# Kernel optimization log

Hardware: AMD Instinct MI355X
Metric: run time of the kernel (lower is better)

Reference implementation:

```python
import jax, jax.numpy as jnp
import numpy as np

B, T, J, D = 64, 800, 50, 200  # batch, context len, query len, 2*hidden

def setup_inputs() -> dict:
    key = jax.random.key(0)
    ks = jax.random.split(key, 8)
    return {
        'h':    jax.random.normal(ks[0], (B, T, D), jnp.float32),
        'u':    jax.random.normal(ks[1], (B, J, D), jnp.float32),
        'w_h':  jax.random.normal(ks[2], (D,), jnp.float32) * 0.05,
        'b_h':  jax.random.normal(ks[3], (1,), jnp.float32) * 0.05,
        'w_u':  jax.random.normal(ks[4], (D,), jnp.float32) * 0.05,
        'b_u':  jax.random.normal(ks[5], (1,), jnp.float32) * 0.05,
        'w_hu': jax.random.normal(ks[6], (D,), jnp.float32) * 0.05,
        'b_hu': jax.random.normal(ks[7], (1,), jnp.float32) * 0.05,
    }

def reference(h, u, w_h, b_h, w_u, b_u, w_hu, b_hu):
    # Similarity: s[b,t,j] = ws_h(h_t) + ws_u(u_j) + ws_hu(h_t * u_j)  (+ summed biases)
    # Computed without materializing the [B,T,J,D] expanded tensors of the original.
    sh = jnp.einsum('btd,d->bt', h, w_h)            # [B,T]
    su = jnp.einsum('bjd,d->bj', u, w_u)            # [B,J]
    shu = jnp.einsum('btd,bjd->btj', h * w_hu, u)   # [B,T,J]
    s = shu + sh[:, :, None] + su[:, None, :] + (b_h + b_u + b_hu)[0]
    # Context-to-query attention
    a = jax.nn.softmax(s, axis=2)                   # [B,T,J]
    c2q = jnp.einsum('btj,bjd->btd', a, u)          # [B,T,D]
    # Query-to-context attention
    b = jax.nn.softmax(jnp.max(s, axis=2), axis=1)  # [B,T]
    q2c = jnp.einsum('bt,btd->bd', b, h)[:, None, :]  # [B,1,D], broadcasts over T
    g = jnp.concatenate([h, c2q, h * c2q, h * q2c], axis=-1)  # [B,T,4D]
    return g
```

## Files before the change

kernel.cpp:

```cpp
#include <hip/hip_runtime.h>
#include <cstdint>
#include <cstddef>

#define B_ 64
#define T_ 800
#define J_ 50
#define D_ 200
#define TILE1 100
#define NTILE1 8
#define NW 8
#define TT 5
#define NPASS 20

__device__ __forceinline__ float dot4(float4 a, float4 b) {
    return fmaf(a.x, b.x, fmaf(a.y, b.y, fmaf(a.z, b.z, a.w * b.w)));
}
__device__ __forceinline__ int rotc(int k, int j) {
    int kk = k + ((j >> 2) & 7);
    return (kk >= 50) ? kk - 50 : kk;
}

__global__ __launch_bounds__(512, 4) void k1_kernel(
    const float* __restrict__ h, const float* __restrict__ u,
    const float* __restrict__ w_h, const float* __restrict__ b_h,
    const float* __restrict__ w_u, const float* __restrict__ b_u,
    const float* __restrict__ w_hu, const float* __restrict__ b_hu,
    float* __restrict__ g, float* __restrict__ smax_ws, float* __restrict__ q2c)
{
    __shared__ __align__(16) float4 u4_s[50][50];
    __shared__ __align__(16) float4 hw_s[NW][TT][25];
    __shared__ float a_s[NW][TT][52];

    const int tid  = threadIdx.x;
    const int b    = blockIdx.x >> 3;
    const int tile = blockIdx.x & 7;

    if (tile == 0 && tid < D_) q2c[b * D_ + tid] = 0.f;

    for (int idx = tid; idx < 2500; idx += 512) {
        const int j = idx / 50, k = idx - (idx / 50) * 50;
        u4_s[j][rotc(k, j)] = *reinterpret_cast<const float4*>(&u[(b * J_ + j) * D_ + 4 * k]);
    }
    __syncthreads();

    const int lane = tid & 63;
    const int w    = tid >> 6;
    const int urow = (lane < 50) ? lane : 49;
    const int dcol = (lane < 50) ? lane : 0;

    float4 whu_r = make_float4(0.f, 0.f, 0.f, 0.f);
    float4 wh_r  = make_float4(0.f, 0.f, 0.f, 0.f);
    if (lane < 50) {
        whu_r = *reinterpret_cast<const float4*>(&w_hu[4 * lane]);
        wh_r  = *reinterpret_cast<const float4*>(&w_h[4 * lane]);
    }

    float su = b_h[0] + b_u[0] + b_hu[0];
    #pragma unroll 5
    for (int k = 0; k < 50; ++k) {
        const float4 wu4 = *reinterpret_cast<const float4*>(&w_u[4 * k]);
        su += dot4(u4_s[urow][rotc(k, urow)], wu4);
    }

    for (int p = w; p < NPASS; p += NW) {
        const int t0 = tile * TILE1 + p * TT;

        float4 h4r[TT];
        float  shr[TT];
        #pragma unroll
        for (int tt = 0; tt < TT; ++tt) {
            float4 h4 = make_float4(0.f, 0.f, 0.f, 0.f);
            if (lane < 50)
                h4 = *reinterpret_cast<const float4*>(&h[(size_t)(b * T_ + t0 + tt) * D_ + 4 * lane]);
            h4r[tt] = h4;
            if (lane < 25) {
                float4 hw; hw.x = h4.x * whu_r.x; hw.y = h4.y * whu_r.y;
                hw.z = h4.z * whu_r.z; hw.w = h4.w * whu_r.w;
                hw_s[w][tt][lane] = hw;
            }
            float ps = dot4(h4, wh_r);
            #pragma unroll
            for (int off = 32; off > 0; off >>= 1) ps += __shfl_xor(ps, off);
            shr[tt] = ps;
        }

        float s[TT];
        #pragma unroll
        for (int tt = 0; tt < TT; ++tt) s[tt] = su + shr[tt];

        #pragma unroll 5
        for (int k = 0; k < 25; ++k) {
            const float4 u4 = u4_s[urow][rotc(k, urow)];
            #pragma unroll
            for (int tt = 0; tt < TT; ++tt) s[tt] += dot4(hw_s[w][tt][k], u4);
        }
        #pragma unroll
        for (int tt = 0; tt < TT; ++tt) {
            if (lane >= 25 && lane < 50) {
                float4 hw; hw.x = h4r[tt].x * whu_r.x; hw.y = h4r[tt].y * whu_r.y;
                hw.z = h4r[tt].z * whu_r.z; hw.w = h4r[tt].w * whu_r.w;
                hw_s[w][tt][lane - 25] = hw;
            }
        }
        #pragma unroll 5
        for (int k = 25; k < 50; ++k) {
            const float4 u4 = u4_s[urow][rotc(k, urow)];
            #pragma unroll
            for (int tt = 0; tt < TT; ++tt) s[tt] += dot4(hw_s[w][tt][k - 25], u4);
        }

        #pragma unroll
        for (int tt = 0; tt < TT; ++tt) {
            float m = (lane < J_) ? s[tt] : -3.4e38f;
            #pragma unroll
            for (int off = 32; off > 0; off >>= 1) m = fmaxf(m, __shfl_xor(m, off));
            float e = (lane < J_) ? __expf(s[tt] - m) : 0.f;
            float sum = e;
            #pragma unroll
            for (int off = 32; off > 0; off >>= 1) sum += __shfl_xor(sum, off);
            if (lane < J_) a_s[w][tt][lane] = e / sum;
            if (lane == 0) smax_ws[b * T_ + (t0 + tt)] = m;
        }

        float4 c2q[TT];
        #pragma unroll
        for (int tt = 0; tt < TT; ++tt) c2q[tt] = make_float4(0.f, 0.f, 0.f, 0.f);
        #pragma unroll 3
        for (int j4 = 0; j4 < 12; ++j4) {
            const float4 ua0 = u4_s[4 * j4 + 0][rotc(dcol, 4 * j4 + 0)];
            const float4 ua1 = u4_s[4 * j4 + 1][rotc(dcol, 4 * j4 + 1)];
            const float4 ua2 = u4_s[4 * j4 + 2][rotc(dcol, 4 * j4 + 2)];
            const float4 ua3 = u4_s[4 * j4 + 3][rotc(dcol, 4 * j4 + 3)];
            #pragma unroll
            for (int tt = 0; tt < TT; ++tt) {
                const float4 a4 = *reinterpret_cast<const float4*>(&a_s[w][tt][4 * j4]);
                c2q[tt].x = fmaf(a4.x, ua0.x, c2q[tt].x);
                c2q[tt].y = fmaf(a4.x, ua0.y, c2q[tt].y);
                c2q[tt].z = fmaf(a4.x, ua0.z, c2q[tt].z);
                c2q[tt].w = fmaf(a4.x, ua0.w, c2q[tt].w);
                c2q[tt].x = fmaf(a4.y, ua1.x, c2q[tt].x);
                c2q[tt].y = fmaf(a4.y, ua1.y, c2q[tt].y);
                c2q[tt].z = fmaf(a4.y, ua1.z, c2q[tt].z);
                c2q[tt].w = fmaf(a4.y, ua1.w, c2q[tt].w);
                c2q[tt].x = fmaf(a4.z, ua2.x, c2q[tt].x);
                c2q[tt].y = fmaf(a4.z, ua2.y, c2q[tt].y);
                c2q[tt].z = fmaf(a4.z, ua2.z, c2q[tt].z);
                c2q[tt].w = fmaf(a4.z, ua2.w, c2q[tt].w);
                c2q[tt].x = fmaf(a4.w, ua3.x, c2q[tt].x);
                c2q[tt].y = fmaf(a4.w, ua3.y, c2q[tt].y);
                c2q[tt].z = fmaf(a4.w, ua3.z, c2q[tt].z);
                c2q[tt].w = fmaf(a4.w, ua3.w, c2q[tt].w);
            }
        }
        {
            const float4 ua0 = u4_s[48][rotc(dcol, 48)];
            const float4 ua1 = u4_s[49][rotc(dcol, 49)];
            #pragma unroll
            for (int tt = 0; tt < TT; ++tt) {
                const float a0 = a_s[w][tt][48], a1 = a_s[w][tt][49];
                c2q[tt].x = fmaf(a0, ua0.x, c2q[tt].x);
                c2q[tt].y = fmaf(a0, ua0.y, c2q[tt].y);
                c2q[tt].z = fmaf(a0, ua0.z, c2q[tt].z);
                c2q[tt].w = fmaf(a0, ua0.w, c2q[tt].w);
                c2q[tt].x = fmaf(a1, ua1.x, c2q[tt].x);
                c2q[tt].y = fmaf(a1, ua1.y, c2q[tt].y);
                c2q[tt].z = fmaf(a1, ua1.z, c2q[tt].z);
                c2q[tt].w = fmaf(a1, ua1.w, c2q[tt].w);
            }
        }

        #pragma unroll
        for (int tt = 0; tt < TT; ++tt) {
            if (lane < 50) {
                const size_t go = (size_t)(b * T_ + t0 + tt) * (4 * D_) + 4 * lane;
                *reinterpret_cast<float4*>(&g[go]) = h4r[tt];
                *reinterpret_cast<float4*>(&g[go + D_]) = c2q[tt];
                float4 hc;
                hc.x = h4r[tt].x * c2q[tt].x; hc.y = h4r[tt].y * c2q[tt].y;
                hc.z = h4r[tt].z * c2q[tt].z; hc.w = h4r[tt].w * c2q[tt].w;
                *reinterpret_cast<float4*>(&g[go + 2 * D_]) = hc;
            }
        }
    }
}

__global__ __launch_bounds__(256) void k3_kernel(const float* __restrict__ h,
                                                 const float* __restrict__ smax,
                                                 float* __restrict__ q2c)
{
    const int b = blockIdx.x >> 3, t8 = blockIdx.x & 7;
    const int rows0 = t8 * 100;
    const int tid = threadIdx.x, lane = tid & 63, w = tid >> 6;
    __shared__ float red[4];
    __shared__ float bs[100];

    float v[4];
    float m = -3.4e38f;
    #pragma unroll
    for (int k = 0; k < 4; ++k) {
        const int t = tid + 256 * k;
        v[k] = (t < T_) ? smax[b * T_ + t] : -3.4e38f;
        m = fmaxf(m, v[k]);
    }
    #pragma unroll
    for (int off = 32; off > 0; off >>= 1) m = fmaxf(m, __shfl_xor(m, off));
    if (lane == 0) red[w] = m;
    __syncthreads();
    m = fmaxf(fmaxf(red[0], red[1]), fmaxf(red[2], red[3]));
    __syncthreads();

    float sum = 0.f;
    #pragma unroll
    for (int k = 0; k < 4; ++k) {
        const int t = tid + 256 * k;
        sum += (t < T_) ? __expf(v[k] - m) : 0.f;
    }
    #pragma unroll
    for (int off = 32; off > 0; off >>= 1) sum += __shfl_xor(sum, off);
    if (lane == 0) red[w] = sum;
    __syncthreads();
    sum = red[0] + red[1] + red[2] + red[3];
    const float inv = 1.f / sum;

    if (tid < 100) bs[tid] = __expf(smax[b * T_ + rows0 + tid] - m) * inv;
    __syncthreads();

    if (tid < D_) {
        const float* hp = h + ((size_t)b * T_ + rows0) * D_ + tid;
        float acc = 0.f;
        #pragma unroll 10
        for (int i = 0; i < 100; ++i) acc = fmaf(bs[i], hp[(size_t)i * D_], acc);
        atomicAdd(&q2c[b * D_ + tid], acc);
    }
}

__global__ __launch_bounds__(256) void k4_kernel(const float* __restrict__ h,
                                                 const float* __restrict__ q2c,
                                                 float* __restrict__ g)
{
    const int b = blockIdx.x >> 4, tc = blockIdx.x & 15;
    const int tid = threadIdx.x;
    if (tid >= 250) return;
    const int tl = tid / 50, d4 = tid - tl * 50;
    const float4 q = *reinterpret_cast<const float4*>(&q2c[b * D_ + 4 * d4]);
    const int trow0 = tc * 50 + tl;
    #pragma unroll 5
    for (int i = 0; i < 10; ++i) {
        const int t = trow0 + 5 * i;
        const float4 h4 = *reinterpret_cast<const float4*>(&h[(size_t)(b * T_ + t) * D_ + 4 * d4]);
        float4 o;
        o.x = h4.x * q.x; o.y = h4.y * q.y; o.z = h4.z * q.z; o.w = h4.w * q.w;
        *reinterpret_cast<float4*>(&g[(size_t)(b * T_ + t) * (4 * D_) + 3 * D_ + 4 * d4]) = o;
    }
}

extern "C" void kernel_launch(void* const* d_in, const int* in_sizes, int n_in,
                              void* d_out, int out_size, void* d_ws, size_t ws_size,
                              hipStream_t stream)
{
    const float* h    = (const float*)d_in[0];
    const float* u    = (const float*)d_in[1];
    const float* w_h  = (const float*)d_in[2];
    const float* b_h  = (const float*)d_in[3];
    const float* w_u  = (const float*)d_in[4];
    const float* b_u  = (const float*)d_in[5];
    const float* w_hu = (const float*)d_in[6];
    const float* b_hu = (const float*)d_in[7];
    float* g = (float*)d_out;

    float* smax = (float*)d_ws;
    float* q2c  = smax + B_ * T_;

    k1_kernel<<<dim3(B_ * NTILE1), dim3(512), 0, stream>>>(h, u, w_h, b_h, w_u, b_u, w_hu, b_hu, g, smax, q2c);
    k3_kernel<<<dim3(B_ * 8), dim3(256), 0, stream>>>(h, smax, q2c);
    k4_kernel<<<dim3(B_ * NTILE1 * 2), dim3(256), 0, stream>>>(h, q2c, g);
}
```

Measured before the change: 276.8 us.

## Give each wave one 10-row pass, reuse hw_s for softmax weights, reload h

k1 now launches 640 threads (10 waves) per block, and each wave handles exactly one 10-row slice of the 100-row tile, so the pass loop and its imbalance (20 passes over 8 waves) go away. The softmax weights are written into the wave's own hw_s region instead of a separate a_s array, which cuts shared memory. h rows are re-read from global/cache instead of being held in registers, which offsets the register pressure from doubling TT. The c2q loop is no longer unrolled. The extra h loads and the higher per-thread accumulator count could hurt latency hiding or cause spills.

```diff
diff --git a/kernel.cpp b/kernel.cpp
--- a/kernel.cpp
+++ b/kernel.cpp
@@ -8,9 +8,8 @@
 #define D_ 200
 #define TILE1 100
 #define NTILE1 8
-#define NW 8
-#define TT 5
-#define NPASS 20
+#define NW 10
+#define TT 10
 
 __device__ __forceinline__ float dot4(float4 a, float4 b) {
     return fmaf(a.x, b.x, fmaf(a.y, b.y, fmaf(a.z, b.z, a.w * b.w)));
@@ -20,7 +19,7 @@
     return (kk >= 50) ? kk - 50 : kk;
 }
 
-__global__ __launch_bounds__(512, 4) void k1_kernel(
+__global__ __launch_bounds__(640, 5) void k1_kernel(
     const float* __restrict__ h, const float* __restrict__ u,
     const float* __restrict__ w_h, const float* __restrict__ b_h,
     const float* __restrict__ w_u, const float* __restrict__ b_u,
@@ -29,7 +28,6 @@
 {
     __shared__ __align__(16) float4 u4_s[50][50];
     __shared__ __align__(16) float4 hw_s[NW][TT][25];
-    __shared__ float a_s[NW][TT][52];
 
     const int tid  = threadIdx.x;
     const int b    = blockIdx.x >> 3;
@@ -37,7 +35,7 @@
 
     if (tile == 0 && tid < D_) q2c[b * D_ + tid] = 0.f;
 
-    for (int idx = tid; idx < 2500; idx += 512) {
+    for (int idx = tid; idx < 2500; idx += 640) {
         const int j = idx / 50, k = idx - (idx / 50) * 50;
         u4_s[j][rotc(k, j)] = *reinterpret_cast<const float4*>(&u[(b * J_ + j) * D_ + 4 * k]);
     }
@@ -62,124 +60,121 @@
         su += dot4(u4_s[urow][rotc(k, urow)], wu4);
     }
 
-    for (int p = w; p < NPASS; p += NW) {
-        const int t0 = tile * TILE1 + p * TT;
-
-        float4 h4r[TT];
-        float  shr[TT];
+    const int t0 = tile * TILE1 + w * TT;
+    const float* hb = h + (size_t)(b * T_ + t0) * D_;
+
+    float s[TT];
+    #pragma unroll
+    for (int tt = 0; tt < TT; ++tt) {
+        float4 h4 = make_float4(0.f, 0.f, 0.f, 0.f);
+        if (lane < 50) h4 = *reinterpret_cast<const float4*>(&hb[(size_t)tt * D_ + 4 * lane]);
+        if (lane < 25) {
+            float4 hw; hw.x = h4.x * whu_r.x; hw.y = h4.y * whu_r.y;
+            hw.z = h4.z * whu_r.z; hw.w = h4.w * whu_r.w;
+            hw_s[w][tt][lane] = hw;
+        }
+        float ps = dot4(h4, wh_r);
+        #pragma unroll
+        for (int off = 32; off > 0; off >>= 1) ps += __shfl_xor(ps, off);
+        s[tt] = su + ps;
+    }
+
+    #pragma unroll 5
+    for (int k = 0; k < 25; ++k) {
+        const float4 u4 = u4_s[urow][rotc(k, urow)];
+        #pragma unroll
+        for (int tt = 0; tt < TT; ++tt) s[tt] += dot4(hw_s[w][tt][k], u4);
+    }
+
+    #pragma unroll
+    for (int tt = 0; tt < TT; ++tt) {
+        if (lane >= 25 && lane < 50) {
+            const float4 h4 = *reinterpret_cast<const float4*>(&hb[(size_t)tt * D_ + 4 * lane]);
+            float4 hw; hw.x = h4.x * whu_r.x; hw.y = h4.y * whu_r.y;
+            hw.z = h4.z * whu_r.z; hw.w = h4.w * whu_r.w;
+            hw_s[w][tt][lane - 25] = hw;
+        }
+    }
+
+    #pragma unroll 5
+    for (int k = 25; k < 50; ++k) {
+        const float4 u4 = u4_s[urow][rotc(k, urow)];
+        #pragma unroll
+        for (int tt = 0; tt < TT; ++tt) s[tt] += dot4(hw_s[w][tt][k - 25], u4);
+    }
+
+    float* a_w = reinterpret_cast<float*>(&hw_s[w][0][0]);
+    #pragma unroll
+    for (int tt = 0; tt < TT; ++tt) {
+        float m = (lane < J_) ? s[tt] : -3.4e38f;
+        #pragma unroll
+        for (int off = 32; off > 0; off >>= 1) m = fmaxf(m, __shfl_xor(m, off));
+        float e = (lane < J_) ? __expf(s[tt] - m) : 0.f;
+        float sum = e;
+        #pragma unroll
+        for (int off = 32; off > 0; off >>= 1) sum += __shfl_xor(sum, off);
+        if (lane < J_) a_w[tt * 52 + lane] = e / sum;
+        if (lane == 0) smax_ws[b * T_ + (t0 + tt)] = m;
+    }
+
+    float4 c2q[TT];
+    #pragma unroll
+    for (int tt = 0; tt < TT; ++tt) c2q[tt] = make_float4(0.f, 0.f, 0.f, 0.f);
+    #pragma unroll 1
+    for (int j4 = 0; j4 < 12; ++j4) {
+        const float4 ua0 = u4_s[4 * j4 + 0][rotc(dcol, 4 * j4 + 0)];
+        const float4 ua1 = u4_s[4 * j4 + 1][rotc(dcol, 4 * j4 + 1)];
+        const float4 ua2 = u4_s[4 * j4 + 2][rotc(dcol, 4 * j4 + 2)];
+        const float4 ua3 = u4_s[4 * j4 + 3][rotc(dcol, 4 * j4 + 3)];
         #pragma unroll
         for (int tt = 0; tt < TT; ++tt) {
-            float4 h4 = make_float4(0.f, 0.f, 0.f, 0.f);
-            if (lane < 50)
-                h4 = *reinterpret_cast<const float4*>(&h[(size_t)(b * T_ + t0 + tt) * D_ + 4 * lane]);
-            h4r[tt] = h4;
-            if (lane < 25) {
-                float4 hw; hw.x = h4.x * whu_r.x; hw.y = h4.y * whu_r.y;
-                hw.z = h4.z * whu_r.z; hw.w = h4.w * whu_r.w;
-                hw_s[w][tt][lane] = hw;
-            }
-            float ps = dot4(h4, wh_r);
-            #pragma unroll
-            for (int off = 32; off > 0; off >>= 1) ps += __shfl_xor(ps, off);
-            shr[tt] = ps;
-        }
-
-        float s[TT];
-        #pragma unroll
-        for (int tt = 0; tt < TT; ++tt) s[tt] = su + shr[tt];
-
-        #pragma unroll 5
-        for (int k = 0; k < 25; ++k) {
-            const float4 u4 = u4_s[urow][rotc(k, urow)];
-            #pragma unroll
-            for (int tt = 0; tt < TT; ++tt) s[tt] += dot4(hw_s[w][tt][k], u4);
-        }
+            const float4 a4 = *reinterpret_cast<const float4*>(&a_w[tt * 52 + 4 * j4]);
+            c2q[tt].x = fmaf(a4.x, ua0.x, c2q[tt].x);
+            c2q[tt].y = fmaf(a4.x, ua0.y, c2q[tt].y);
+            c2q[tt].z = fmaf(a4.x, ua0.z, c2q[tt].z);
+            c2q[tt].w = fmaf(a4.x, ua0.w, c2q[tt].w);
+            c2q[tt].x = fmaf(a4.y, ua1.x, c2q[tt].x);
+            c2q[tt].y = fmaf(a4.y, ua1.y, c2q[tt].y);
+            c2q[tt].z = fmaf(a4.y, ua1.z, c2q[tt].z);
+            c2q[tt].w = fmaf(a4.y, ua1.w, c2q[tt].w);
+            c2q[tt].x = fmaf(a4.z, ua2.x, c2q[tt].x);
+            c2q[tt].y = fmaf(a4.z, ua2.y, c2q[tt].y);
+            c2q[tt].z = fmaf(a4.z, ua2.z, c2q[tt].z);
+            c2q[tt].w = fmaf(a4.z, ua2.w, c2q[tt].w);
+            c2q[tt].x = fmaf(a4.w, ua3.x, c2q[tt].x);
+            c2q[tt].y = fmaf(a4.w, ua3.y, c2q[tt].y);
+            c2q[tt].z = fmaf(a4.w, ua3.z, c2q[tt].z);
+            c2q[tt].w = fmaf(a4.w, ua3.w, c2q[tt].w);
+        }
+    }
+    {
+        const float4 ua0 = u4_s[48][rotc(dcol, 48)];
+        const float4 ua1 = u4_s[49][rotc(dcol, 49)];
         #pragma unroll
         for (int tt = 0; tt < TT; ++tt) {
-            if (lane >= 25 && lane < 50) {
-                float4 hw; hw.x = h4r[tt].x * whu_r.x; hw.y = h4r[tt].y * whu_r.y;
-                hw.z = h4r[tt].z * whu_r.z; hw.w = h4r[tt].w * whu_r.w;
-                hw_s[w][tt][lane - 25] = hw;
-            }
-        }
-        #pragma unroll 5
-        for (int k = 25; k < 50; ++k) {
-            const float4 u4 = u4_s[urow][rotc(k, urow)];
-            #pragma unroll
-            for (int tt = 0; tt < TT; ++tt) s[tt] += dot4(hw_s[w][tt][k - 25], u4);
-        }
-
-        #pragma unroll
-        for (int tt = 0; tt < TT; ++tt) {
-            float m = (lane < J_) ? s[tt] : -3.4e38f;
-            #pragma unroll
-            for (int off = 32; off > 0; off >>= 1) m = fmaxf(m, __shfl_xor(m, off));
-            float e = (lane < J_) ? __expf(s[tt] - m) : 0.f;
-            float sum = e;
-            #pragma unroll
-            for (int off = 32; off > 0; off >>= 1) sum += __shfl_xor(sum, off);
-            if (lane < J_) a_s[w][tt][lane] = e / sum;
-            if (lane == 0) smax_ws[b * T_ + (t0 + tt)] = m;
-        }
-
-        float4 c2q[TT];
-        #pragma unroll
-        for (int tt = 0; tt < TT; ++tt) c2q[tt] = make_float4(0.f, 0.f, 0.f, 0.f);
-        #pragma unroll 3
-        for (int j4 = 0; j4 < 12; ++j4) {
-            const float4 ua0 = u4_s[4 * j4 + 0][rotc(dcol, 4 * j4 + 0)];
-            const float4 ua1 = u4_s[4 * j4 + 1][rotc(dcol, 4 * j4 + 1)];
-            const float4 ua2 = u4_s[4 * j4 + 2][rotc(dcol, 4 * j4 + 2)];
-            const float4 ua3 = u4_s[4 * j4 + 3][rotc(dcol, 4 * j4 + 3)];
-            #pragma unroll
-            for (int tt = 0; tt < TT; ++tt) {
-                const float4 a4 = *reinterpret_cast<const float4*>(&a_s[w][tt][4 * j4]);
-                c2q[tt].x = fmaf(a4.x, ua0.x, c2q[tt].x);
-                c2q[tt].y = fmaf(a4.x, ua0.y, c2q[tt].y);
-                c2q[tt].z = fmaf(a4.x, ua0.z, c2q[tt].z);
-                c2q[tt].w = fmaf(a4.x, ua0.w, c2q[tt].w);
-                c2q[tt].x = fmaf(a4.y, ua1.x, c2q[tt].x);
-                c2q[tt].y = fmaf(a4.y, ua1.y, c2q[tt].y);
-                c2q[tt].z = fmaf(a4.y, ua1.z, c2q[tt].z);
-                c2q[tt].w = fmaf(a4.y, ua1.w, c2q[tt].w);
-                c2q[tt].x = fmaf(a4.z, ua2.x, c2q[tt].x);
-                c2q[tt].y = fmaf(a4.z, ua2.y, c2q[tt].y);
-                c2q[tt].z = fmaf(a4.z, ua2.z, c2q[tt].z);
-                c2q[tt].w = fmaf(a4.z, ua2.w, c2q[tt].w);
-                c2q[tt].x = fmaf(a4.w, ua3.x, c2q[tt].x);
-                c2q[tt].y = fmaf(a4.w, ua3.y, c2q[tt].y);
-                c2q[tt].z = fmaf(a4.w, ua3.z, c2q[tt].z);
-                c2q[tt].w = fmaf(a4.w, ua3.w, c2q[tt].w);
-            }
-        }
-        {
-            const float4 ua0 = u4_s[48][rotc(dcol, 48)];
-            const float4 ua1 = u4_s[49][rotc(dcol, 49)];
-            #pragma unroll
-            for (int tt = 0; tt < TT; ++tt) {
-                const float a0 = a_s[w][tt][48], a1 = a_s[w][tt][49];
-                c2q[tt].x = fmaf(a0, ua0.x, c2q[tt].x);
-                c2q[tt].y = fmaf(a0, ua0.y, c2q[tt].y);
-                c2q[tt].z = fmaf(a0, ua0.z, c2q[tt].z);
-                c2q[tt].w = fmaf(a0, ua0.w, c2q[tt].w);
-                c2q[tt].x = fmaf(a1, ua1.x, c2q[tt].x);
-                c2q[tt].y = fmaf(a1, ua1.y, c2q[tt].y);
-                c2q[tt].z = fmaf(a1, ua1.z, c2q[tt].z);
-                c2q[tt].w = fmaf(a1, ua1.w, c2q[tt].w);
-            }
-        }
-
-        #pragma unroll
-        for (int tt = 0; tt < TT; ++tt) {
-            if (lane < 50) {
-                const size_t go = (size_t)(b * T_ + t0 + tt) * (4 * D_) + 4 * lane;
-                *reinterpret_cast<float4*>(&g[go]) = h4r[tt];
-                *reinterpret_cast<float4*>(&g[go + D_]) = c2q[tt];
-                float4 hc;
-                hc.x = h4r[tt].x * c2q[tt].x; hc.y = h4r[tt].y * c2q[tt].y;
-                hc.z = h4r[tt].z * c2q[tt].z; hc.w = h4r[tt].w * c2q[tt].w;
-                *reinterpret_cast<float4*>(&g[go + 2 * D_]) = hc;
-            }
+            const float a0 = a_w[tt * 52 + 48], a1 = a_w[tt * 52 + 49];
+            c2q[tt].x = fmaf(a0, ua0.x, c2q[tt].x);
+            c2q[tt].y = fmaf(a0, ua0.y, c2q[tt].y);
+            c2q[tt].z = fmaf(a0, ua0.z, c2q[tt].z);
+            c2q[tt].w = fmaf(a0, ua0.w, c2q[tt].w);
+            c2q[tt].x = fmaf(a1, ua1.x, c2q[tt].x);
+            c2q[tt].y = fmaf(a1, ua1.y, c2q[tt].y);
+            c2q[tt].z = fmaf(a1, ua1.z, c2q[tt].z);
+            c2q[tt].w = fmaf(a1, ua1.w, c2q[tt].w);
+        }
+    }
+
+    #pragma unroll
+    for (int tt = 0; tt < TT; ++tt) {
+        if (lane < 50) {
+            const float4 h4 = *reinterpret_cast<const float4*>(&hb[(size_t)tt * D_ + 4 * lane]);
+            const size_t go = (size_t)(b * T_ + t0 + tt) * (4 * D_) + 4 * lane;
+            *reinterpret_cast<float4*>(&g[go]) = h4;
+            *reinterpret_cast<float4*>(&g[go + D_]) = c2q[tt];
+            float4 hc;
+            hc.x = h4.x * c2q[tt].x; hc.y = h4.y * c2q[tt].y;
+            hc.z = h4.z * c2q[tt].z; hc.w = h4.w * c2q[tt].w;
+            *reinterpret_cast<float4*>(&g[go + 2 * D_]) = hc;
         }
     }
 }
@@ -271,7 +266,7 @@
     float* smax = (float*)d_ws;
     float* q2c  = smax + B_ * T_;
 
-    k1_kernel<<<dim3(B_ * NTILE1), dim3(512), 0, stream>>>(h, u, w_h, b_h, w_u, b_u, w_hu, b_hu, g, smax, q2c);
+    k1_kernel<<<dim3(B_ * NTILE1), dim3(640), 0, stream>>>(h, u, w_h, b_h, w_u, b_u, w_hu, b_hu, g, smax, q2c);
     k3_kernel<<<dim3(B_ * 8), dim3(256), 0, stream>>>(h, smax, q2c);
     k4_kernel<<<dim3(B_ * NTILE1 * 2), dim3(256), 0, stream>>>(h, q2c, g);
 }
```

After: 292.9 us. 1.06x slower.
